# Kernel optimization log

Hardware: AMD Instinct MI355X
Metric: run time of the kernel (lower is better)

Reference implementation:

```python
import jax, jax.numpy as jnp
import numpy as np

B, C, L, E = 5888, 128, 16, 10   # nodes, channels, sum(2l+1), num elements
P3, P2, P1 = 23, 4, 1            # num coupling paths per correlation order


def _sparse_u(key, shape, density=0.05):
    # U matrices are Clebsch-Gordan-derived and highly sparse
    k1, k2 = jax.random.split(key)
    vals = jax.random.normal(k1, shape, dtype=jnp.float32)
    mask = (jax.random.uniform(k2, shape) < density).astype(jnp.float32)
    return vals * mask


def setup_inputs() -> dict:
    key = jax.random.key(0)
    ks = jax.random.split(key, 8)
    x = jax.random.normal(ks[0], (B, C, L), dtype=jnp.float32)      # node features
    y = jax.random.uniform(ks[1], (B, E), dtype=jnp.float32)        # element one-hot (relaxed)
    U3 = _sparse_u(ks[2], (L, L, L, P3))
    U2 = _sparse_u(ks[3], (L, L, P2))
    U1 = _sparse_u(ks[4], (L, P1))
    w3 = jax.random.normal(ks[5], (E, P3, C), dtype=jnp.float32) / P3
    w2 = jax.random.normal(ks[6], (E, P2, C), dtype=jnp.float32) / P2
    w1 = jax.random.normal(ks[7], (E, P1, C), dtype=jnp.float32) / P1
    return {"x": x, "y": y, "U3": U3, "U2": U2, "U1": U1,
            "w3": w3, "w2": w2, "w1": w1}


def reference(x, y, U3, U2, U1, w3, w2, w1):
    # --- main contraction (nu = correlation = 3, irrep_out lmax=0) ---
    # 'wxik,ekc,bci,be->bcwx'
    out = jnp.einsum('wxik,ekc,bci,be->bcwx', U3, w3, x, y, optimize=True)  # [B,C,L,L]
    # --- nu = 2: weighting then feature contraction ---
    c = jnp.einsum('wxk,ekc,be->bcwx', U2, w2, y, optimize=True) + out      # [B,C,L,L]
    out = jnp.einsum('bcwi,bci->bcw', c, x)                                  # [B,C,L]
    # --- nu = 1 ---
    c = jnp.einsum('wk,ekc,be->bcw', U1, w1, y, optimize=True) + out        # [B,C,L]
    out = jnp.einsum('bci,bci->bc', c, x)                                    # [B,C]
    return out.reshape(out.shape[0], -1)
```

## Files before the change

### kernel.cpp

```cpp
#include <hip/hip_runtime.h>
#include <utility>

using u16 = unsigned short;
using u32 = unsigned int;

typedef float  f32x4  __attribute__((ext_vector_type(4)));
typedef __bf16 bf16x8 __attribute__((ext_vector_type(8)));

#define DI __device__ __forceinline__

struct RepT { unsigned char a, b, c, t; };
struct Tables4 {
  RepT rep[248];
  RepT slotmono[992];
  int n3, n2, n1;
};

constexpr int csort3key(int w, int x, int i) {
  int a = w, b = x, c = i, t = 0;
  if (a > b) { t = a; a = b; b = t; }
  if (b > c) { t = b; b = c; c = t; }
  if (a > b) { t = a; a = b; b = t; }
  return (a << 8) | (b << 4) | c;
}

constexpr Tables4 build_tables4() {
  Tables4 T = {};
  bool used3[4096] = {};
  bool used2[256] = {};
  int nr = 0;
  for (int a = 0; a < 16; a++) for (int b = a; b < 16; b++) for (int c = b; c < 16; c++) {
    const int key = (a << 8) | (b << 4) | c;
    bool canon = true;
    for (int q = 1; q < 4; q++)
      if (csort3key((a + 4 * q) & 15, (b + 4 * q) & 15, (c + 4 * q) & 15) < key) canon = false;
    if (!canon) continue;
    for (int q = 0; q < 4; q++) {
      const int kk = csort3key((a + 4 * q) & 15, (b + 4 * q) & 15, (c + 4 * q) & 15);
      if (!used3[kk]) {
        used3[kk] = true;
        const int f = (nr >> 3) * 32 + q * 8 + (nr & 7);
        T.slotmono[f].a = (unsigned char)(kk >> 8);
        T.slotmono[f].b = (unsigned char)((kk >> 4) & 15);
        T.slotmono[f].c = (unsigned char)(kk & 15);
        T.slotmono[f].t = 3;
      }
    }
    T.rep[nr].a = (unsigned char)a; T.rep[nr].b = (unsigned char)b;
    T.rep[nr].c = (unsigned char)c; T.rep[nr].t = 3; nr++;
  }
  T.n3 = nr;
  for (int a = 0; a < 16; a++) for (int b = a; b < 16; b++) {
    const int key = (a << 4) | b;
    bool canon = true;
    for (int q = 1; q < 4; q++) {
      int aa = (a + 4 * q) & 15, bb = (b + 4 * q) & 15;
      if (aa > bb) { int t = aa; aa = bb; bb = t; }
      if (((aa << 4) | bb) < key) canon = false;
    }
    if (!canon) continue;
    for (int q = 0; q < 4; q++) {
      int aa = (a + 4 * q) & 15, bb = (b + 4 * q) & 15;
      if (aa > bb) { int t = aa; aa = bb; bb = t; }
      const int kk = (aa << 4) | bb;
      if (!used2[kk]) {
        used2[kk] = true;
        const int f = (nr >> 3) * 32 + q * 8 + (nr & 7);
        T.slotmono[f].a = (unsigned char)(kk >> 4);
        T.slotmono[f].b = (unsigned char)(kk & 15);
        T.slotmono[f].c = 0;
        T.slotmono[f].t = 2;
      }
    }
    T.rep[nr].a = (unsigned char)a; T.rep[nr].b = (unsigned char)b;
    T.rep[nr].c = 0; T.rep[nr].t = 2; nr++;
  }
  T.n2 = nr;
  for (int a = 0; a < 4; a++) {
    for (int q = 0; q < 4; q++) {
      const int f = (nr >> 3) * 32 + q * 8 + (nr & 7);
      T.slotmono[f].a = (unsigned char)((a + 4 * q) & 15);
      T.slotmono[f].b = 0; T.slotmono[f].c = 0; T.slotmono[f].t = 1;
    }
    T.rep[nr].a = (unsigned char)a; T.rep[nr].b = 0; T.rep[nr].c = 0;
    T.rep[nr].t = 1; nr++;
  }
  T.n1 = nr;
  for (; nr < 248; nr++) { T.rep[nr].a = 0; T.rep[nr].b = 0; T.rep[nr].c = 0; T.rep[nr].t = 0; }
  return T;
}

constexpr Tables4 TT4 = build_tables4();
static_assert(TT4.n3 == 204, "cubic rep count");
static_assert(TT4.n2 == 240, "quad rep count");
static_assert(TT4.n1 == 244, "linear rep count");

__device__ const Tables4 g_T4 = build_tables4();

#define BN 5888
#define CN 128
#define EN 10
#define NCHUNK 31
#define NPATH 32

DI u16 f2bf(float f) { union { __bf16 h; u16 s; } u; u.h = (__bf16)f; return u.s; }
DI float bf2f(u16 v) { union { u32 u; float f; } w; w.u = ((u32)v) << 16; return w.f; }

#define PREP_THREADS (NCHUNK * 2 * 64 * 8)

__global__ void prep_kernel(const float* __restrict__ U3, const float* __restrict__ U2,
                            const float* __restrict__ U1, u16* __restrict__ Sfrag16) {
  const int tid = blockIdx.x * 256 + threadIdx.x;
  if (tid >= PREP_THREADS) return;
  const int j = tid & 7, l = (tid >> 3) & 63, cp = tid >> 9;
  const int chunk = cp >> 1, P = cp & 1;
  const int path = P * 16 + (l & 15), q = l >> 4;
  const RepT m = g_T4.slotmono[chunk * 32 + q * 8 + j];
  float v = 0.f;
  if (m.t == 3 && path < 23) {
    const int a = m.a, b = m.b, d = m.c;
    v = U3[((a * 16 + b) * 16 + d) * 23 + path];
    if (a == b && b == d) {
    } else if (a == b) {
      v += U3[((a * 16 + d) * 16 + a) * 23 + path]
         + U3[((d * 16 + a) * 16 + a) * 23 + path];
    } else if (b == d) {
      v += U3[((b * 16 + a) * 16 + b) * 23 + path]
         + U3[((b * 16 + b) * 16 + a) * 23 + path];
    } else {
      v += U3[((a * 16 + d) * 16 + b) * 23 + path]
         + U3[((b * 16 + a) * 16 + d) * 23 + path]
         + U3[((b * 16 + d) * 16 + a) * 23 + path]
         + U3[((d * 16 + a) * 16 + b) * 23 + path]
         + U3[((d * 16 + b) * 16 + a) * 23 + path];
    }
  } else if (m.t == 2 && path >= 23 && path < 27) {
    const int k = path - 23, a = m.a, b = m.b;
    v = U2[(a * 16 + b) * 4 + k];
    if (a != b) v += U2[(b * 16 + a) * 4 + k];
  } else if (m.t == 1 && path == 27) {
    v = U1[m.a];
  }
  Sfrag16[tid] = f2bf(v);
}

template<int R>
DI float featf(const float* xr) {
  constexpr RepT rp = TT4.rep[R];
  if constexpr (rp.t == 3) return xr[rp.a] * xr[rp.b] * xr[rp.c];
  else if constexpr (rp.t == 2) return xr[rp.a] * xr[rp.b];
  else if constexpr (rp.t == 1) return xr[rp.a];
  else return 0.f;
}

template<int C>
DI bf16x8 make_B(const float* xr) {
  bf16x8 r;
  r[0] = (__bf16)featf<C * 8 + 0>(xr);
  r[1] = (__bf16)featf<C * 8 + 1>(xr);
  r[2] = (__bf16)featf<C * 8 + 2>(xr);
  r[3] = (__bf16)featf<C * 8 + 3>(xr);
  r[4] = (__bf16)featf<C * 8 + 4>(xr);
  r[5] = (__bf16)featf<C * 8 + 5>(xr);
  r[6] = (__bf16)featf<C * 8 + 6>(xr);
  r[7] = (__bf16)featf<C * 8 + 7>(xr);
  return r;
}

template<int C>
DI void chunk_step(const uint4* sfl, const float* xr, f32x4& a0, f32x4& a1) {
  const bf16x8 B = make_B<C>(xr);
  const bf16x8 A0 = *reinterpret_cast<const bf16x8*>(sfl + (C * 2 + 0) * 64);
  const bf16x8 A1 = *reinterpret_cast<const bf16x8*>(sfl + (C * 2 + 1) * 64);
  a0 = __builtin_amdgcn_mfma_f32_16x16x32_bf16(A0, B, a0, 0, 0, 0);
  a1 = __builtin_amdgcn_mfma_f32_16x16x32_bf16(A1, B, a1, 0, 0, 0);
}

template<int... Cs>
DI void all_chunks(std::integer_sequence<int, Cs...>, const uint4* sfl,
                   const float* xr, f32x4& a0, f32x4& a1) {
  (chunk_step<Cs>(sfl, xr, a0, a1), ...);
}

DI void load_xr(const float* __restrict__ x, int pair, int q, float* xr) {
  const float* base = x + pair * 16;
#pragma unroll
  for (int u = 0; u < 4; u++) {
    const int g = (u + q) & 3;
    const float4 v = *(const float4*)(base + g * 4);
    xr[u * 4 + 0] = v.x;
    xr[u * 4 + 1] = v.y;
    xr[u * 4 + 2] = v.z;
    xr[u * 4 + 3] = v.w;
  }
}

__global__ __launch_bounds__(1024) void main_kernel(
    const float* __restrict__ x, const float* __restrict__ y,
    const float* __restrict__ w3, const float* __restrict__ w2, const float* __restrict__ w1,
    const uint4* __restrict__ Sfrag, float* __restrict__ out)
{
  __shared__ uint4 sfrag[NCHUNK * 2 * 64];
  __shared__ u16  wbl[2][32 * 128];
  const int tid = threadIdx.x;

  for (int idx = tid; idx < NCHUNK * 2 * 64; idx += 1024) sfrag[idx] = Sfrag[idx];

  const int nl = tid >> 9;
  const int bnode = blockIdx.x * 2 + nl;
  {
    const int t  = tid & 511;
    const int p  = t >> 4;
    const int c0 = (t & 15) * 8;
    float yv[EN];
#pragma unroll
    for (int e = 0; e < EN; e++) yv[e] = y[bnode * EN + e];
    float acc[8];
#pragma unroll
    for (int m = 0; m < 8; m++) acc[m] = 0.f;
    const float* wsrc = nullptr; int stride = 0;
    if (p < 23)       { wsrc = w3 + p * 128;        stride = 23 * 128; }
    else if (p < 27)  { wsrc = w2 + (p - 23) * 128; stride = 4 * 128; }
    else if (p == 27) { wsrc = w1;                  stride = 128; }
    if (wsrc) {
      for (int e = 0; e < EN; e++) {
        const float* src = wsrc + e * stride + c0;
        const float4 v0 = *(const float4*)(src);
        const float4 v1 = *(const float4*)(src + 4);
        acc[0] += yv[e] * v0.x; acc[1] += yv[e] * v0.y;
        acc[2] += yv[e] * v0.z; acc[3] += yv[e] * v0.w;
        acc[4] += yv[e] * v1.x; acc[5] += yv[e] * v1.y;
        acc[6] += yv[e] * v1.z; acc[7] += yv[e] * v1.w;
      }
    }
#pragma unroll
    for (int m = 0; m < 8; m++) wbl[nl][p * 128 + c0 + m] = f2bf(acc[m]);
  }
  __syncthreads();

  const int wn = (tid >> 6) & 7, lane = tid & 63;
  const int q = lane >> 4, n = lane & 15;
  const int pair0 = bnode * 128 + wn * 16 + n;

  float xr[16];
  load_xr(x, pair0, q, xr);

  const uint4* sfl = sfrag + lane;
  f32x4 a0 = {0.f, 0.f, 0.f, 0.f};
  f32x4 a1 = a0;
  all_chunks(std::make_integer_sequence<int, NCHUNK>{}, sfl, xr, a0, a1);

  const int cc = wn * 16 + n;
  float p0 = 0.f;
#pragma unroll
  for (int rg = 0; rg < 4; rg++) {
    p0 += a0[rg] * bf2f(wbl[nl][(q * 4 + rg) * 128 + cc]);
    p0 += a1[rg] * bf2f(wbl[nl][(16 + q * 4 + rg) * 128 + cc]);
  }
  p0 += __shfl_xor(p0, 16);
  p0 += __shfl_xor(p0, 32);
  if (q == 0) out[pair0] = p0;
}

extern "C" void kernel_launch(void* const* d_in, const int* in_sizes, int n_in,
                              void* d_out, int out_size, void* d_ws, size_t ws_size,
                              hipStream_t stream) {
  const float* x  = (const float*)d_in[0];
  const float* y  = (const float*)d_in[1];
  const float* U3 = (const float*)d_in[2];
  const float* U2 = (const float*)d_in[3];
  const float* U1 = (const float*)d_in[4];
  const float* w3 = (const float*)d_in[5];
  const float* w2 = (const float*)d_in[6];
  const float* w1 = (const float*)d_in[7];
  u16*   Sfrag16 = (u16*)d_ws;
  float* out     = (float*)d_out;

  hipLaunchKernelGGL(prep_kernel, dim3((PREP_THREADS + 255) / 256), dim3(256), 0, stream,
                     U3, U2, U1, Sfrag16);
  hipLaunchKernelGGL(main_kernel, dim3(BN / 2), dim3(1024), 0, stream,
                     x, y, w3, w2, w1, (const uint4*)d_ws, out);
}
```

Before: 193.7 us.

## Split chunk contraction across two blocks per node with atomic accumulation

Each node is now handled by two 512-thread blocks instead of packing two nodes into one 1024-thread block. The two blocks split the 31 MFMA chunks 16/15, and each stages only its half of the U fragments in shared memory. This shortens the per-wave serial MFMA chain, cuts LDS per block and raises block count and occupancy. In exchange, each block recomputes the element-weighted w tables and reloads x, the output needs a memset plus atomicAdd, and float atomics make the summation order nondeterministic.

```diff
diff --git a/kernel.cpp b/kernel.cpp
--- a/kernel.cpp
+++ b/kernel.cpp
@@ -102,6 +102,8 @@
 #define EN 10
 #define NCHUNK 31
 #define NPATH 32
+#define H0 16
+#define H1 15
 
 DI u16 f2bf(float f) { union { __bf16 h; u16 s; } u; u.h = (__bf16)f; return u.s; }
 DI float bf2f(u16 v) { union { u32 u; float f; } w; w.u = ((u32)v) << 16; return w.f; }
@@ -167,19 +169,19 @@
   return r;
 }
 
-template<int C>
+template<int C, int CB>
 DI void chunk_step(const uint4* sfl, const float* xr, f32x4& a0, f32x4& a1) {
   const bf16x8 B = make_B<C>(xr);
-  const bf16x8 A0 = *reinterpret_cast<const bf16x8*>(sfl + (C * 2 + 0) * 64);
-  const bf16x8 A1 = *reinterpret_cast<const bf16x8*>(sfl + (C * 2 + 1) * 64);
+  const bf16x8 A0 = *reinterpret_cast<const bf16x8*>(sfl + ((C - CB) * 2 + 0) * 64);
+  const bf16x8 A1 = *reinterpret_cast<const bf16x8*>(sfl + ((C - CB) * 2 + 1) * 64);
   a0 = __builtin_amdgcn_mfma_f32_16x16x32_bf16(A0, B, a0, 0, 0, 0);
   a1 = __builtin_amdgcn_mfma_f32_16x16x32_bf16(A1, B, a1, 0, 0, 0);
 }
 
-template<int... Cs>
-DI void all_chunks(std::integer_sequence<int, Cs...>, const uint4* sfl,
+template<int CB, int... Cs>
+DI void run_chunks(std::integer_sequence<int, Cs...>, const uint4* sfl,
                    const float* xr, f32x4& a0, f32x4& a1) {
-  (chunk_step<Cs>(sfl, xr, a0, a1), ...);
+  (chunk_step<CB + Cs, CB>(sfl, xr, a0, a1), ...);
 }
 
 DI void load_xr(const float* __restrict__ x, int pair, int q, float* xr) {
@@ -195,26 +197,27 @@
   }
 }
 
-__global__ __launch_bounds__(1024) void main_kernel(
+__global__ __launch_bounds__(512) void main_kernel(
     const float* __restrict__ x, const float* __restrict__ y,
     const float* __restrict__ w3, const float* __restrict__ w2, const float* __restrict__ w1,
     const uint4* __restrict__ Sfrag, float* __restrict__ out)
 {
-  __shared__ uint4 sfrag[NCHUNK * 2 * 64];
-  __shared__ u16  wbl[2][32 * 128];
+  __shared__ uint4 sfrag[H0 * 2 * 64];
+  __shared__ u16  wbl[28 * 128];
   const int tid = threadIdx.x;
-
-  for (int idx = tid; idx < NCHUNK * 2 * 64; idx += 1024) sfrag[idx] = Sfrag[idx];
-
-  const int nl = tid >> 9;
-  const int bnode = blockIdx.x * 2 + nl;
+  const int half = blockIdx.x & 1;
+  const int node = blockIdx.x >> 1;
+
+  const int nfrag = half ? (H1 * 2 * 64) : (H0 * 2 * 64);
+  const uint4* srcS = Sfrag + (half ? (H0 * 2 * 64) : 0);
+  for (int idx = tid; idx < nfrag; idx += 512) sfrag[idx] = srcS[idx];
+
   {
-    const int t  = tid & 511;
-    const int p  = t >> 4;
-    const int c0 = (t & 15) * 8;
+    const int p  = tid >> 4;
+    const int c0 = (tid & 15) * 8;
     float yv[EN];
 #pragma unroll
-    for (int e = 0; e < EN; e++) yv[e] = y[bnode * EN + e];
+    for (int e = 0; e < EN; e++) yv[e] = y[node * EN + e];
     float acc[8];
 #pragma unroll
     for (int m = 0; m < 8; m++) acc[m] = 0.f;
@@ -233,14 +236,16 @@
         acc[6] += yv[e] * v1.z; acc[7] += yv[e] * v1.w;
       }
     }
-#pragma unroll
-    for (int m = 0; m < 8; m++) wbl[nl][p * 128 + c0 + m] = f2bf(acc[m]);
+    if (p < 28) {
+#pragma unroll
+      for (int m = 0; m < 8; m++) wbl[p * 128 + c0 + m] = f2bf(acc[m]);
+    }
   }
   __syncthreads();
 
-  const int wn = (tid >> 6) & 7, lane = tid & 63;
+  const int wn = tid >> 6, lane = tid & 63;
   const int q = lane >> 4, n = lane & 15;
-  const int pair0 = bnode * 128 + wn * 16 + n;
+  const int pair0 = node * 128 + wn * 16 + n;
 
   float xr[16];
   load_xr(x, pair0, q, xr);
@@ -248,18 +253,22 @@
   const uint4* sfl = sfrag + lane;
   f32x4 a0 = {0.f, 0.f, 0.f, 0.f};
   f32x4 a1 = a0;
-  all_chunks(std::make_integer_sequence<int, NCHUNK>{}, sfl, xr, a0, a1);
+  if (half == 0)
+    run_chunks<0>(std::make_integer_sequence<int, H0>{}, sfl, xr, a0, a1);
+  else
+    run_chunks<H0>(std::make_integer_sequence<int, H1>{}, sfl, xr, a0, a1);
 
   const int cc = wn * 16 + n;
   float p0 = 0.f;
 #pragma unroll
-  for (int rg = 0; rg < 4; rg++) {
-    p0 += a0[rg] * bf2f(wbl[nl][(q * 4 + rg) * 128 + cc]);
-    p0 += a1[rg] * bf2f(wbl[nl][(16 + q * 4 + rg) * 128 + cc]);
+  for (int rg = 0; rg < 4; rg++) p0 += a0[rg] * bf2f(wbl[(q * 4 + rg) * 128 + cc]);
+  if (q < 3) {
+#pragma unroll
+    for (int rg = 0; rg < 4; rg++) p0 += a1[rg] * bf2f(wbl[(16 + q * 4 + rg) * 128 + cc]);
   }
   p0 += __shfl_xor(p0, 16);
   p0 += __shfl_xor(p0, 32);
-  if (q == 0) out[pair0] = p0;
+  if (q == 0) atomicAdd(&out[pair0], p0);
 }
 
 extern "C" void kernel_launch(void* const* d_in, const int* in_sizes, int n_in,
@@ -276,8 +285,9 @@
   u16*   Sfrag16 = (u16*)d_ws;
   float* out     = (float*)d_out;
 
+  hipMemsetAsync(out, 0, out_size, stream);
   hipLaunchKernelGGL(prep_kernel, dim3((PREP_THREADS + 255) / 256), dim3(256), 0, stream,
                      U3, U2, U1, Sfrag16);
-  hipLaunchKernelGGL(main_kernel, dim3(BN / 2), dim3(1024), 0, stream,
+  hipLaunchKernelGGL(main_kernel, dim3(BN * 2), dim3(512), 0, stream,
                      x, y, w3, w2, w1, (const uint4*)d_ws, out);
 }
```

Measured after the change: 227.8 us. +17.6%, slower.

## Switch to 32x32x16 MFMA with two-way cyclic symmetry packing of monomials

Applied to the files above, without the earlier changes.

Replaces the pair of 16x16x32 bf16 MFMAs per chunk with a single 32x32x16 MFMA covering all 32 paths. The monomial table moves from 4-way to 2-way cyclic shift symmetry, so each lane half holds an 8-shifted copy of x, giving 61 K-chunks of 16 instead of 31 of 32. Blocks shrink to 512 threads, each wave now handling 32 channels. The intent is fewer instructions per MAC and better occupancy. In exchange it adds more feature computations per lane (more chunks of scalar products).

```diff
diff --git a/kernel.cpp b/kernel.cpp
--- a/kernel.cpp
+++ b/kernel.cpp
@@ -4,15 +4,16 @@
 using u16 = unsigned short;
 using u32 = unsigned int;
 
-typedef float  f32x4  __attribute__((ext_vector_type(4)));
-typedef __bf16 bf16x8 __attribute__((ext_vector_type(8)));
+typedef float  f32x4   __attribute__((ext_vector_type(4)));
+typedef float  f32x16  __attribute__((ext_vector_type(16)));
+typedef __bf16 bf16x8  __attribute__((ext_vector_type(8)));
 
 #define DI __device__ __forceinline__
 
 struct RepT { unsigned char a, b, c, t; };
-struct Tables4 {
-  RepT rep[248];
-  RepT slotmono[992];
+struct Tables8 {
+  RepT rep[488];
+  RepT slotmono[976];
   int n3, n2, n1;
 };
 
@@ -23,23 +24,22 @@
   if (a > b) { t = a; a = b; b = t; }
   return (a << 8) | (b << 4) | c;
 }
-
-constexpr Tables4 build_tables4() {
-  Tables4 T = {};
+constexpr int csort2key(int a, int b) { return a <= b ? ((a << 4) | b) : ((b << 4) | a); }
+
+constexpr Tables8 build_tables8() {
+  Tables8 T = {};
   bool used3[4096] = {};
   bool used2[256] = {};
   int nr = 0;
   for (int a = 0; a < 16; a++) for (int b = a; b < 16; b++) for (int c = b; c < 16; c++) {
-    const int key = (a << 8) | (b << 4) | c;
-    bool canon = true;
-    for (int q = 1; q < 4; q++)
-      if (csort3key((a + 4 * q) & 15, (b + 4 * q) & 15, (c + 4 * q) & 15) < key) canon = false;
-    if (!canon) continue;
-    for (int q = 0; q < 4; q++) {
-      const int kk = csort3key((a + 4 * q) & 15, (b + 4 * q) & 15, (c + 4 * q) & 15);
+    const int key  = (a << 8) | (b << 4) | c;
+    const int rkey = csort3key((a + 8) & 15, (b + 8) & 15, (c + 8) & 15);
+    if (rkey < key) continue;
+    for (int q = 0; q < 2; q++) {
+      const int kk = q ? rkey : key;
       if (!used3[kk]) {
         used3[kk] = true;
-        const int f = (nr >> 3) * 32 + q * 8 + (nr & 7);
+        const int f = (nr >> 3) * 16 + q * 8 + (nr & 7);
         T.slotmono[f].a = (unsigned char)(kk >> 8);
         T.slotmono[f].b = (unsigned char)((kk >> 4) & 15);
         T.slotmono[f].c = (unsigned char)(kk & 15);
@@ -51,21 +51,14 @@
   }
   T.n3 = nr;
   for (int a = 0; a < 16; a++) for (int b = a; b < 16; b++) {
-    const int key = (a << 4) | b;
-    bool canon = true;
-    for (int q = 1; q < 4; q++) {
-      int aa = (a + 4 * q) & 15, bb = (b + 4 * q) & 15;
-      if (aa > bb) { int t = aa; aa = bb; bb = t; }
-      if (((aa << 4) | bb) < key) canon = false;
-    }
-    if (!canon) continue;
-    for (int q = 0; q < 4; q++) {
-      int aa = (a + 4 * q) & 15, bb = (b + 4 * q) & 15;
-      if (aa > bb) { int t = aa; aa = bb; bb = t; }
-      const int kk = (aa << 4) | bb;
+    const int key  = (a << 4) | b;
+    const int rkey = csort2key((a + 8) & 15, (b + 8) & 15);
+    if (rkey < key) continue;
+    for (int q = 0; q < 2; q++) {
+      const int kk = q ? rkey : key;
       if (!used2[kk]) {
         used2[kk] = true;
-        const int f = (nr >> 3) * 32 + q * 8 + (nr & 7);
+        const int f = (nr >> 3) * 16 + q * 8 + (nr & 7);
         T.slotmono[f].a = (unsigned char)(kk >> 4);
         T.slotmono[f].b = (unsigned char)(kk & 15);
         T.slotmono[f].c = 0;
@@ -76,46 +69,43 @@
     T.rep[nr].c = 0; T.rep[nr].t = 2; nr++;
   }
   T.n2 = nr;
-  for (int a = 0; a < 4; a++) {
-    for (int q = 0; q < 4; q++) {
-      const int f = (nr >> 3) * 32 + q * 8 + (nr & 7);
-      T.slotmono[f].a = (unsigned char)((a + 4 * q) & 15);
+  for (int a = 0; a < 8; a++) {
+    for (int q = 0; q < 2; q++) {
+      const int f = (nr >> 3) * 16 + q * 8 + (nr & 7);
+      T.slotmono[f].a = (unsigned char)((a + 8 * q) & 15);
       T.slotmono[f].b = 0; T.slotmono[f].c = 0; T.slotmono[f].t = 1;
     }
     T.rep[nr].a = (unsigned char)a; T.rep[nr].b = 0; T.rep[nr].c = 0;
     T.rep[nr].t = 1; nr++;
   }
   T.n1 = nr;
-  for (; nr < 248; nr++) { T.rep[nr].a = 0; T.rep[nr].b = 0; T.rep[nr].c = 0; T.rep[nr].t = 0; }
   return T;
 }
 
-constexpr Tables4 TT4 = build_tables4();
-static_assert(TT4.n3 == 204, "cubic rep count");
-static_assert(TT4.n2 == 240, "quad rep count");
-static_assert(TT4.n1 == 244, "linear rep count");
-
-__device__ const Tables4 g_T4 = build_tables4();
+constexpr Tables8 TT8 = build_tables8();
+static_assert(TT8.n3 == 408, "cubic rep count");
+static_assert(TT8.n2 == 480, "quad rep count");
+static_assert(TT8.n1 == 488, "linear rep count");
+
+__device__ const Tables8 g_T8 = build_tables8();
 
 #define BN 5888
 #define CN 128
 #define EN 10
-#define NCHUNK 31
-#define NPATH 32
+#define NCHUNK 61
 
 DI u16 f2bf(float f) { union { __bf16 h; u16 s; } u; u.h = (__bf16)f; return u.s; }
 DI float bf2f(u16 v) { union { u32 u; float f; } w; w.u = ((u32)v) << 16; return w.f; }
 
-#define PREP_THREADS (NCHUNK * 2 * 64 * 8)
+#define PREP_THREADS (NCHUNK * 64 * 8)
 
 __global__ void prep_kernel(const float* __restrict__ U3, const float* __restrict__ U2,
                             const float* __restrict__ U1, u16* __restrict__ Sfrag16) {
   const int tid = blockIdx.x * 256 + threadIdx.x;
   if (tid >= PREP_THREADS) return;
-  const int j = tid & 7, l = (tid >> 3) & 63, cp = tid >> 9;
-  const int chunk = cp >> 1, P = cp & 1;
-  const int path = P * 16 + (l & 15), q = l >> 4;
-  const RepT m = g_T4.slotmono[chunk * 32 + q * 8 + j];
+  const int j = tid & 7, l = (tid >> 3) & 63, chunk = tid >> 9;
+  const int path = l & 31, q = l >> 5;
+  const RepT m = g_T8.slotmono[chunk * 16 + q * 8 + j];
   float v = 0.f;
   if (m.t == 3 && path < 23) {
     const int a = m.a, b = m.b, d = m.c;
@@ -146,7 +136,7 @@
 
 template<int R>
 DI float featf(const float* xr) {
-  constexpr RepT rp = TT4.rep[R];
+  constexpr RepT rp = TT8.rep[R];
   if constexpr (rp.t == 3) return xr[rp.a] * xr[rp.b] * xr[rp.c];
   else if constexpr (rp.t == 2) return xr[rp.a] * xr[rp.b];
   else if constexpr (rp.t == 1) return xr[rp.a];
@@ -168,25 +158,23 @@
 }
 
 template<int C>
-DI void chunk_step(const uint4* sfl, const float* xr, f32x4& a0, f32x4& a1) {
+DI void chunk_step(const uint4* sfl, const float* xr, f32x16& acc) {
   const bf16x8 B = make_B<C>(xr);
-  const bf16x8 A0 = *reinterpret_cast<const bf16x8*>(sfl + (C * 2 + 0) * 64);
-  const bf16x8 A1 = *reinterpret_cast<const bf16x8*>(sfl + (C * 2 + 1) * 64);
-  a0 = __builtin_amdgcn_mfma_f32_16x16x32_bf16(A0, B, a0, 0, 0, 0);
-  a1 = __builtin_amdgcn_mfma_f32_16x16x32_bf16(A1, B, a1, 0, 0, 0);
+  const bf16x8 A = *reinterpret_cast<const bf16x8*>(sfl + C * 64);
+  acc = __builtin_amdgcn_mfma_f32_32x32x16_bf16(A, B, acc, 0, 0, 0);
 }
 
 template<int... Cs>
-DI void all_chunks(std::integer_sequence<int, Cs...>, const uint4* sfl,
-                   const float* xr, f32x4& a0, f32x4& a1) {
-  (chunk_step<Cs>(sfl, xr, a0, a1), ...);
+DI void run_chunks(std::integer_sequence<int, Cs...>, const uint4* sfl,
+                   const float* xr, f32x16& acc) {
+  (chunk_step<Cs>(sfl, xr, acc), ...);
 }
 
 DI void load_xr(const float* __restrict__ x, int pair, int q, float* xr) {
   const float* base = x + pair * 16;
 #pragma unroll
   for (int u = 0; u < 4; u++) {
-    const int g = (u + q) & 3;
+    const int g = (u + 2 * q) & 3;
     const float4 v = *(const float4*)(base + g * 4);
     xr[u * 4 + 0] = v.x;
     xr[u * 4 + 1] = v.y;
@@ -195,29 +183,30 @@
   }
 }
 
-__global__ __launch_bounds__(1024) void main_kernel(
+__global__ __launch_bounds__(512, 4) void main_kernel(
     const float* __restrict__ x, const float* __restrict__ y,
     const float* __restrict__ w3, const float* __restrict__ w2, const float* __restrict__ w1,
     const uint4* __restrict__ Sfrag, float* __restrict__ out)
 {
-  __shared__ uint4 sfrag[NCHUNK * 2 * 64];
+  __shared__ uint4 sfrag[NCHUNK * 64];
   __shared__ u16  wbl[2][32 * 128];
   const int tid = threadIdx.x;
-
-  for (int idx = tid; idx < NCHUNK * 2 * 64; idx += 1024) sfrag[idx] = Sfrag[idx];
-
-  const int nl = tid >> 9;
-  const int bnode = blockIdx.x * 2 + nl;
+  const int node0 = blockIdx.x * 2;
+
+  for (int idx = tid; idx < NCHUNK * 64; idx += 512) sfrag[idx] = Sfrag[idx];
+
+  const int nl = tid >> 8;
+  const int bnode = node0 + nl;
   {
-    const int t  = tid & 511;
-    const int p  = t >> 4;
-    const int c0 = (t & 15) * 8;
+    const int tl = tid & 255;
+    const int p  = tl >> 3;
+    const int c0 = (tl & 7) * 16;
     float yv[EN];
 #pragma unroll
     for (int e = 0; e < EN; e++) yv[e] = y[bnode * EN + e];
-    float acc[8];
-#pragma unroll
-    for (int m = 0; m < 8; m++) acc[m] = 0.f;
+    float acc[16];
+#pragma unroll
+    for (int m = 0; m < 16; m++) acc[m] = 0.f;
     const float* wsrc = nullptr; int stride = 0;
     if (p < 23)       { wsrc = w3 + p * 128;        stride = 23 * 128; }
     else if (p < 27)  { wsrc = w2 + (p - 23) * 128; stride = 4 * 128; }
@@ -227,37 +216,42 @@
         const float* src = wsrc + e * stride + c0;
         const float4 v0 = *(const float4*)(src);
         const float4 v1 = *(const float4*)(src + 4);
-        acc[0] += yv[e] * v0.x; acc[1] += yv[e] * v0.y;
-        acc[2] += yv[e] * v0.z; acc[3] += yv[e] * v0.w;
-        acc[4] += yv[e] * v1.x; acc[5] += yv[e] * v1.y;
-        acc[6] += yv[e] * v1.z; acc[7] += yv[e] * v1.w;
+        const float4 v2 = *(const float4*)(src + 8);
+        const float4 v3 = *(const float4*)(src + 12);
+        acc[0]  += yv[e] * v0.x; acc[1]  += yv[e] * v0.y;
+        acc[2]  += yv[e] * v0.z; acc[3]  += yv[e] * v0.w;
+        acc[4]  += yv[e] * v1.x; acc[5]  += yv[e] * v1.y;
+        acc[6]  += yv[e] * v1.z; acc[7]  += yv[e] * v1.w;
+        acc[8]  += yv[e] * v2.x; acc[9]  += yv[e] * v2.y;
+        acc[10] += yv[e] * v2.z; acc[11] += yv[e] * v2.w;
+        acc[12] += yv[e] * v3.x; acc[13] += yv[e] * v3.y;
+        acc[14] += yv[e] * v3.z; acc[15] += yv[e] * v3.w;
       }
     }
 #pragma unroll
-    for (int m = 0; m < 8; m++) wbl[nl][p * 128 + c0 + m] = f2bf(acc[m]);
+    for (int m = 0; m < 16; m++) wbl[nl][p * 128 + c0 + m] = f2bf(acc[m]);
   }
   __syncthreads();
 
-  const int wn = (tid >> 6) & 7, lane = tid & 63;
-  const int q = lane >> 4, n = lane & 15;
-  const int pair0 = bnode * 128 + wn * 16 + n;
+  const int w = tid >> 6, wn = w & 3;
+  const int lane = tid & 63, col = lane & 31, q = lane >> 5;
+  const int pair0 = bnode * 128 + wn * 32 + col;
 
   float xr[16];
   load_xr(x, pair0, q, xr);
 
   const uint4* sfl = sfrag + lane;
-  f32x4 a0 = {0.f, 0.f, 0.f, 0.f};
-  f32x4 a1 = a0;
-  all_chunks(std::make_integer_sequence<int, NCHUNK>{}, sfl, xr, a0, a1);
-
-  const int cc = wn * 16 + n;
+  f32x16 acc = {0.f, 0.f, 0.f, 0.f, 0.f, 0.f, 0.f, 0.f,
+                0.f, 0.f, 0.f, 0.f, 0.f, 0.f, 0.f, 0.f};
+  run_chunks(std::make_integer_sequence<int, NCHUNK>{}, sfl, xr, acc);
+
+  const int cc = wn * 32 + col;
   float p0 = 0.f;
 #pragma unroll
-  for (int rg = 0; rg < 4; rg++) {
-    p0 += a0[rg] * bf2f(wbl[nl][(q * 4 + rg) * 128 + cc]);
-    p0 += a1[rg] * bf2f(wbl[nl][(16 + q * 4 + rg) * 128 + cc]);
-  }
-  p0 += __shfl_xor(p0, 16);
+  for (int r = 0; r < 16; r++) {
+    const int row = (r & 3) + 8 * (r >> 2) + 4 * q;
+    p0 += acc[r] * bf2f(wbl[nl][row * 128 + cc]);
+  }
   p0 += __shfl_xor(p0, 32);
   if (q == 0) out[pair0] = p0;
 }
@@ -276,8 +270,8 @@
   u16*   Sfrag16 = (u16*)d_ws;
   float* out     = (float*)d_out;
 
-  hipLaunchKernelGGL(prep_kernel, dim3((PREP_THREADS + 255) / 256), dim3(256), 0, stream,
+  hipLaunchKernelGGL(prep_kernel, dim3(PREP_THREADS / 256), dim3(256), 0, stream,
                      U3, U2, U1, Sfrag16);
-  hipLaunchKernelGGL(main_kernel, dim3(BN / 2), dim3(1024), 0, stream,
+  hipLaunchKernelGGL(main_kernel, dim3(BN / 2), dim3(512), 0, stream,
                      x, y, w3, w2, w1, (const uint4*)d_ws, out);
 }
```

Measured after the change: 179.1 us. 7.5% less time.
